# Kernel tuning notes

Measured on AMD Instinct MI355X. Metric: run time of the kernel, lower is better.

## Reference

```python
import jax, jax.numpy as jnp
import numpy as np

# Hyperparameters from init_kwargs
SIGMA = 0.01   # memristor conductance noise std
R = 1.0        # line resistance scale used in power accounting
WMAX1 = 1.0
WMAX2 = 1.0
B, C, H, W = 4, 3, 64, 64
K = 2                      # AvgPool2d kernel/stride
D1 = C * (H // K) * (W // K)   # 3072 flattened features after pooling
D2 = 2048
D3 = 1024


def setup_inputs() -> dict:
    key = jax.random.key(0)
    ks = jax.random.split(key, 4)
    x = jax.random.normal(ks[0], (B, C, H, W), jnp.float32)
    bias = jax.random.normal(ks[1], (C, H, W), jnp.float32) * 0.01
    W1 = jax.random.normal(ks[2], (D2, D1), jnp.float32) / np.float32(np.sqrt(D1))
    W2 = jax.random.normal(ks[3], (D3, D2), jnp.float32) / np.float32(np.sqrt(D2))
    g1 = jnp.float32(1.0)  # learnt_Gmax[0], initialized to Wmax[0]
    g2 = jnp.float32(1.0)  # learnt_Gmax[1]
    return {"x": x, "bias": bias, "W1": W1, "W2": W2, "g1": g1, "g2": g2}


def reference(x, bias, W1, W2, g1, g2):
    # input bias (MemSE.input_bias=True)
    x = x + bias[None]
    b = x.shape[0]
    eye2 = jnp.eye(D2, dtype=x.dtype)
    eye3 = jnp.eye(D3, dtype=x.dtype)

    # --- AvgPool2d(2,2): gamma is still empty at this point, only mean pooled ---
    x = x.reshape(b, C, H // K, K, W // K, K).mean(axis=(3, 5))
    x = x.reshape(b, -1)                        # [B, D1]

    # --- Linear 1: crossbar noise injection (gamma empty -> created here) ---
    c1 = g1 / WMAX1                             # conductance scaling G = c * W
    mu = x @ W1.T                               # [B, D2] mean propagation
    m2 = x * x                                  # E[x^2] (gamma == 0 before this layer)
    # two conductance arrays (pos/neg) each with iid noise var sigma^2, output /c
    vn1 = 2.0 * (SIGMA / c1) ** 2 * jnp.sum(m2, axis=-1)        # [B]
    gamma = vn1[:, None, None] * eye2[None]                      # [B, D2, D2]
    P_tot = (c1 / R) * jnp.einsum('oi,bi->b', jnp.abs(W1), m2)   # crossbar power

    # --- Softplus: first-order moment propagation (Jacobian = sigmoid(mu)) ---
    d = jax.nn.sigmoid(mu)                      # [B, D2]
    gamma = gamma * d[:, :, None] * d[:, None, :]
    mu = jax.nn.softplus(mu)

    # --- Linear 2: full covariance propagation W gamma W^T + noise diag ---
    c2 = g2 / WMAX2
    mu2 = mu @ W2.T                             # [B, D3]
    tmp = jnp.einsum('oi,bij->boj', W2, gamma)  # [B, D3, D2]
    gamma2 = jnp.einsum('boj,pj->bop', tmp, W2) # [B, D3, D3]
    m2b = mu * mu + jnp.diagonal(gamma, axis1=1, axis2=2)        # E[x^2]
    vn2 = 2.0 * (SIGMA / c2) ** 2 * jnp.sum(m2b, axis=-1)
    gamma2 = gamma2 + vn2[:, None, None] * eye3[None]
    P_tot = P_tot + (c2 / R) * jnp.einsum('oi,bi->b', jnp.abs(W2), m2b)

    return mu2, gamma2, P_tot
```

## Files before the change

### kernel.cpp

```cpp
#include <hip/hip_runtime.h>
#include <hip/hip_bf16.h>
#include <cstdint>

#define SIGMA 0.01f

constexpr int D1 = 3072;
constexpr int D2 = 2048;
constexpr int D3 = 1024;

typedef __bf16 bf16x8 __attribute__((ext_vector_type(8)));
typedef float f32x4 __attribute__((ext_vector_type(4)));

#define GLOAD16(gp, lp) \
  __builtin_amdgcn_global_load_lds((const __attribute__((address_space(1))) void*)(gp), \
                                   (__attribute__((address_space(3))) void*)(lp), 16, 0, 0)

__global__ void pool_kernel(const float* __restrict__ x, const float* __restrict__ bias,
                            float* __restrict__ pooled, float* __restrict__ Spart) {
  int idx = blockIdx.x * 256 + threadIdx.x;
  int b = idx / D1;
  int r = idx % D1;
  int c = r >> 10;
  int oh = (r >> 5) & 31;
  int ow = r & 31;
  int xb = ((b * 3 + c) * 64 + oh * 2) * 64 + ow * 2;
  int bb = (c * 64 + oh * 2) * 64 + ow * 2;
  float v = 0.25f * ((x[xb] + bias[bb]) + (x[xb + 1] + bias[bb + 1]) +
                     (x[xb + 64] + bias[bb + 64]) + (x[xb + 65] + bias[bb + 65]));
  pooled[idx] = v;
  float s = v * v;
  #pragma unroll
  for (int off = 32; off; off >>= 1) s += __shfl_down(s, off, 64);
  __shared__ float wsum[4];
  if ((threadIdx.x & 63) == 0) wsum[threadIdx.x >> 6] = s;
  __syncthreads();
  if (threadIdx.x == 0) Spart[blockIdx.x] = wsum[0] + wsum[1] + wsum[2] + wsum[3];
}

__global__ void lin1_kernel(const float* __restrict__ pooled, const float* __restrict__ W1,
                            const float* __restrict__ Spart, const float* __restrict__ g1p,
                            float* __restrict__ musp, float* __restrict__ dscale,
                            float* __restrict__ m2b, float* __restrict__ Pp1) {
  int o = blockIdx.x, tid = threadIdx.x;
  const float4* wrow = (const float4*)(W1 + (size_t)o * D1);
  const float4* p4 = (const float4*)pooled;
  float acc[4] = {0, 0, 0, 0}, pab[4] = {0, 0, 0, 0};
  #pragma unroll
  for (int it = 0; it < 3; it++) {
    int i4 = tid + it * 256;
    float4 w = wrow[i4];
    float ax = fabsf(w.x), ay = fabsf(w.y), az = fabsf(w.z), aw2 = fabsf(w.w);
    #pragma unroll
    for (int b = 0; b < 4; b++) {
      float4 p = p4[b * 768 + i4];
      acc[b] += w.x * p.x + w.y * p.y + w.z * p.z + w.w * p.w;
      pab[b] += ax * p.x * p.x + ay * p.y * p.y + az * p.z * p.z + aw2 * p.w * p.w;
    }
  }
  __shared__ float red[8][4];
  #pragma unroll
  for (int v = 0; v < 8; v++) {
    float s = (v < 4) ? acc[v] : pab[v - 4];
    #pragma unroll
    for (int off = 32; off; off >>= 1) s += __shfl_down(s, off, 64);
    if ((tid & 63) == 0) red[v][tid >> 6] = s;
  }
  __syncthreads();
  if (tid < 8) {
    float s = red[tid][0] + red[tid][1] + red[tid][2] + red[tid][3];
    if (tid < 4) {
      int b = tid;
      float ss = 0.f;
      #pragma unroll
      for (int i = 0; i < 12; i++) ss += Spart[b * 12 + i];
      float c1 = g1p[0];
      float vn1 = 2.0f * (SIGMA / c1) * (SIGMA / c1) * ss;
      float d = 1.0f / (1.0f + expf(-s));
      float sp = fmaxf(s, 0.f) + log1pf(expf(-fabsf(s)));
      musp[b * D2 + o] = sp;
      dscale[b * D2 + o] = sqrtf(vn1) * d;
      m2b[b * D2 + o] = sp * sp + vn1 * d * d;
    } else {
      Pp1[(size_t)(tid - 4) * D2 + o] = s;
    }
  }
}

__global__ void lin2_prep_kernel(const float* __restrict__ W2, const float* __restrict__ musp,
                                 const float* __restrict__ dscale, const float* __restrict__ m2b,
                                 __bf16* __restrict__ E, float* __restrict__ mu2,
                                 float* __restrict__ Pp2) {
  int o = blockIdx.x, tid = threadIdx.x;
  const float* wrow = W2 + (size_t)o * D2;
  int j0 = tid * 8;
  float w[8];
  *(float4*)&w[0] = *(const float4*)(wrow + j0);
  *(float4*)&w[4] = *(const float4*)(wrow + j0 + 4);
  float acc[4], pab[4];
  #pragma unroll
  for (int b = 0; b < 4; b++) {
    const float* ms = musp + b * D2 + j0;
    const float* dsc = dscale + b * D2 + j0;
    const float* mb = m2b + b * D2 + j0;
    bf16x8 ev;
    float a = 0.f, p = 0.f;
    #pragma unroll
    for (int jj = 0; jj < 8; jj++) {
      ev[jj] = (__bf16)(w[jj] * dsc[jj]);
      a += w[jj] * ms[jj];
      p += fabsf(w[jj]) * mb[jj];
    }
    *(bf16x8*)(E + ((size_t)b * D3 + o) * D2 + j0) = ev;
    acc[b] = a;
    pab[b] = p;
  }
  __shared__ float red[8][4];
  #pragma unroll
  for (int v = 0; v < 8; v++) {
    float s = (v < 4) ? acc[v] : pab[v - 4];
    #pragma unroll
    for (int off = 32; off; off >>= 1) s += __shfl_down(s, off, 64);
    if ((tid & 63) == 0) red[v][tid >> 6] = s;
  }
  __syncthreads();
  if (tid < 8) {
    float s = red[tid][0] + red[tid][1] + red[tid][2] + red[tid][3];
    if (tid < 4) mu2[tid * D3 + o] = s;
    else Pp2[(size_t)(tid - 4) * D3 + o] = s;
  }
}

__global__ void scalars_kernel(const float* __restrict__ m2b, const float* __restrict__ Pp1,
                               const float* __restrict__ Pp2, const float* __restrict__ g1p,
                               const float* __restrict__ g2p, float* __restrict__ vn2v,
                               float* __restrict__ Ptot) {
  int b = blockIdx.x, tid = threadIdx.x;
  float sm = 0.f, s1 = 0.f, s2 = 0.f;
  #pragma unroll
  for (int i = 0; i < 8; i++) {
    sm += m2b[(size_t)b * D2 + tid + i * 256];
    s1 += Pp1[(size_t)b * D2 + tid + i * 256];
  }
  #pragma unroll
  for (int i = 0; i < 4; i++) s2 += Pp2[(size_t)b * D3 + tid + i * 256];
  __shared__ float red[3][4];
  #pragma unroll
  for (int v = 0; v < 3; v++) {
    float s = (v == 0) ? sm : (v == 1) ? s1 : s2;
    #pragma unroll
    for (int off = 32; off; off >>= 1) s += __shfl_down(s, off, 64);
    if ((tid & 63) == 0) red[v][tid >> 6] = s;
  }
  __syncthreads();
  if (tid == 0) {
    float c2 = g2p[0];
    float smt = red[0][0] + red[0][1] + red[0][2] + red[0][3];
    float s1t = red[1][0] + red[1][1] + red[1][2] + red[1][3];
    float s2t = red[2][0] + red[2][1] + red[2][2] + red[2][3];
    vn2v[b] = 2.0f * (SIGMA / c2) * (SIGMA / c2) * smt;
    Ptot[b] = g1p[0] * s1t + c2 * s2t;
  }
}

__global__ __launch_bounds__(256, 4) void gamma2_gemm(const __bf16* __restrict__ E,
                                                      const float* __restrict__ vn2v,
                                                      float* __restrict__ gamma2) {
  int bid = blockIdx.x, tid = threadIdx.x;
  int wid = tid >> 6, lane = tid & 63;
  int wr = wid >> 1, wc = wid & 1;

  int xcd = bid & 7, r = bid >> 3;
  int b = xcd >> 1;
  int tm = ((xcd & 1) << 3) | (r & 7);
  int tn = r >> 3;

  __shared__ __bf16 As[2][4096], Bs[2][4096];
  char* AsB = (char*)As;
  char* BsB = (char*)Bs;

  const __bf16* Eb = E + (size_t)b * D3 * D2;
  int rb0 = wid >> 1, ks0 = wid & 1;
  int rb1 = (wid + 4) >> 1, ks1 = wid & 1;
  int srow = lane >> 2, skc = lane & 3;
  const __bf16* gA0 = Eb + (size_t)(tm * 64 + rb0 * 16 + srow) * D2 + ks0 * 32 + skc * 8;
  const __bf16* gA1 = Eb + (size_t)(tm * 64 + rb1 * 16 + srow) * D2 + ks1 * 32 + skc * 8;
  const __bf16* gB0 = Eb + (size_t)(tn * 64 + rb0 * 16 + srow) * D2 + ks0 * 32 + skc * 8;
  const __bf16* gB1 = Eb + (size_t)(tn * 64 + rb1 * 16 + srow) * D2 + ks1 * 32 + skc * 8;
  unsigned dst0 = (unsigned)wid * 1024u;
  unsigned dst1 = dst0 + 4096u;

  int fr = lane & 15, kg = lane >> 4;
  unsigned po = (unsigned)(fr * 64 + kg * 16);
  unsigned aM0 = (unsigned)(wr * 4096) + po;
  unsigned aM1 = aM0 + 2048u;
  unsigned bN0 = (unsigned)(wc * 4096) + po;
  unsigned bN1 = bN0 + 2048u;

  f32x4 acc[2][2] = {};

#define STAGE(bufoff, kelem)                                   \
  {                                                            \
    GLOAD16(gA0 + (kelem), AsB + (bufoff) + dst0);             \
    GLOAD16(gA1 + (kelem), AsB + (bufoff) + dst1);             \
    GLOAD16(gB0 + (kelem), BsB + (bufoff) + dst0);             \
    GLOAD16(gB1 + (kelem), BsB + (bufoff) + dst1);             \
  }

#define COMPUTE(bufoff)                                                         \
  {                                                                             \
    _Pragma("unroll")                                                           \
    for (int ks2 = 0; ks2 < 2; ks2++) {                                         \
      unsigned kso = (unsigned)ks2 << 10;                                       \
      bf16x8 a0 = *(const bf16x8*)(AsB + (bufoff) + aM0 + kso);                 \
      bf16x8 a1 = *(const bf16x8*)(AsB + (bufoff) + aM1 + kso);                 \
      bf16x8 b0 = *(const bf16x8*)(BsB + (bufoff) + bN0 + kso);                 \
      bf16x8 b1 = *(const bf16x8*)(BsB + (bufoff) + bN1 + kso);                 \
      acc[0][0] = __builtin_amdgcn_mfma_f32_16x16x32_bf16(a0, b0, acc[0][0], 0, 0, 0); \
      acc[0][1] = __builtin_amdgcn_mfma_f32_16x16x32_bf16(a0, b1, acc[0][1], 0, 0, 0); \
      acc[1][0] = __builtin_amdgcn_mfma_f32_16x16x32_bf16(a1, b0, acc[1][0], 0, 0, 0); \
      acc[1][1] = __builtin_amdgcn_mfma_f32_16x16x32_bf16(a1, b1, acc[1][1], 0, 0, 0); \
    }                                                                           \
  }

  STAGE(0u, 0);
  __syncthreads();
  unsigned cur = 0;
  #pragma unroll 1
  for (int kt = 0; kt < 31; kt++) {
    unsigned nxt = cur ^ 8192u;
    STAGE(nxt, (kt + 1) * 64);
    COMPUTE(cur);
    __syncthreads();
    cur = nxt;
  }
  COMPUTE(cur);
#undef STAGE
#undef COMPUTE

  float vn2 = vn2v[b];
  float* outb = gamma2 + (size_t)b * D3 * D3;
  int row0 = tm * 64 + wr * 32 + kg * 4;
  int col0 = tn * 64 + wc * 32 + fr;
  #pragma unroll
  for (int mi = 0; mi < 2; mi++)
    #pragma unroll
    for (int ni = 0; ni < 2; ni++)
      #pragma unroll
      for (int rg = 0; rg < 4; rg++) {
        int row = row0 + mi * 16 + rg;
        int cc = col0 + ni * 16;
        float v = acc[mi][ni][rg];
        if (row == cc) v += vn2;
        outb[(size_t)row * D3 + cc] = v;
      }
}

extern "C" void kernel_launch(void* const* d_in, const int* in_sizes, int n_in,
                              void* d_out, int out_size, void* d_ws, size_t ws_size,
                              hipStream_t stream) {
  (void)in_sizes; (void)n_in; (void)out_size; (void)ws_size;
  const float* x    = (const float*)d_in[0];
  const float* bias = (const float*)d_in[1];
  const float* W1   = (const float*)d_in[2];
  const float* W2   = (const float*)d_in[3];
  const float* g1   = (const float*)d_in[4];
  const float* g2   = (const float*)d_in[5];
  float* out = (float*)d_out;

  float* ws     = (float*)d_ws;
  float* pooled = ws;
  float* musp   = pooled + 4 * D1;
  float* dscale = musp + 4 * D2;
  float* m2b    = dscale + 4 * D2;
  float* Pp1    = m2b + 4 * D2;
  float* Pp2    = Pp1 + 4 * D2;
  float* Spart  = Pp2 + 4 * D3;
  float* vn2v   = Spart + 48;
  size_t used = (size_t)(4 * D1 + 4 * 4 * D2 + 4 * D3 + 64) * 4;
  size_t eoff = (used + 255) / 256 * 256;
  __bf16* E = (__bf16*)((char*)d_ws + eoff);

  float* mu2_out  = out;
  float* gam_out  = out + 4 * D3;
  float* ptot_out = out + 4 * D3 + (size_t)4 * D3 * D3;

  pool_kernel<<<48, 256, 0, stream>>>(x, bias, pooled, Spart);
  lin1_kernel<<<2048, 256, 0, stream>>>(pooled, W1, Spart, g1, musp, dscale, m2b, Pp1);
  lin2_prep_kernel<<<1024, 256, 0, stream>>>(W2, musp, dscale, m2b, E, mu2_out, Pp2);
  scalars_kernel<<<4, 256, 0, stream>>>(m2b, Pp1, Pp2, g1, g2, vn2v, ptot_out);
  gamma2_gemm<<<1024, 256, 0, stream>>>(E, vn2v, gam_out);
}
```

Measured before the change: 57.99 us.

## Exploit gamma2 symmetry to compute only upper-triangle tiles; process two rows per block

The covariance GEMM now launches only the upper-triangular 64x64 tiles per batch (136 of 256), decoding tile indices via an inverse triangular-number mapping. Each off-diagonal tile also writes its transposed copy, roughly halving the MFMA work and E-operand loads. In addition, lin1 and lin2_prep each handle two output rows per block, so pooled and activation vectors are reused across rows and fewer blocks are launched. The transposed stores are column-strided float4 writes, which may coalesce poorly.

```diff
diff --git a/kernel.cpp b/kernel.cpp
--- a/kernel.cpp
+++ b/kernel.cpp
@@ -41,35 +41,42 @@
                             const float* __restrict__ Spart, const float* __restrict__ g1p,
                             float* __restrict__ musp, float* __restrict__ dscale,
                             float* __restrict__ m2b, float* __restrict__ Pp1) {
-  int o = blockIdx.x, tid = threadIdx.x;
-  const float4* wrow = (const float4*)(W1 + (size_t)o * D1);
+  int o2 = blockIdx.x << 1, tid = threadIdx.x;
+  const float4* w0p = (const float4*)(W1 + (size_t)o2 * D1);
+  const float4* w1p = (const float4*)(W1 + (size_t)(o2 + 1) * D1);
   const float4* p4 = (const float4*)pooled;
-  float acc[4] = {0, 0, 0, 0}, pab[4] = {0, 0, 0, 0};
+  float a0[4] = {0,0,0,0}, q0[4] = {0,0,0,0}, a1[4] = {0,0,0,0}, q1[4] = {0,0,0,0};
   #pragma unroll
   for (int it = 0; it < 3; it++) {
     int i4 = tid + it * 256;
-    float4 w = wrow[i4];
-    float ax = fabsf(w.x), ay = fabsf(w.y), az = fabsf(w.z), aw2 = fabsf(w.w);
+    float4 w0 = w0p[i4], w1 = w1p[i4];
+    float x0x = fabsf(w0.x), x0y = fabsf(w0.y), x0z = fabsf(w0.z), x0w = fabsf(w0.w);
+    float x1x = fabsf(w1.x), x1y = fabsf(w1.y), x1z = fabsf(w1.z), x1w = fabsf(w1.w);
     #pragma unroll
     for (int b = 0; b < 4; b++) {
       float4 p = p4[b * 768 + i4];
-      acc[b] += w.x * p.x + w.y * p.y + w.z * p.z + w.w * p.w;
-      pab[b] += ax * p.x * p.x + ay * p.y * p.y + az * p.z * p.z + aw2 * p.w * p.w;
+      float px = p.x * p.x, py = p.y * p.y, pz = p.z * p.z, pw = p.w * p.w;
+      a0[b] += w0.x * p.x + w0.y * p.y + w0.z * p.z + w0.w * p.w;
+      q0[b] += x0x * px + x0y * py + x0z * pz + x0w * pw;
+      a1[b] += w1.x * p.x + w1.y * p.y + w1.z * p.z + w1.w * p.w;
+      q1[b] += x1x * px + x1y * py + x1z * pz + x1w * pw;
     }
   }
-  __shared__ float red[8][4];
-  #pragma unroll
-  for (int v = 0; v < 8; v++) {
-    float s = (v < 4) ? acc[v] : pab[v - 4];
+  __shared__ float red[16][4];
+  #pragma unroll
+  for (int v = 0; v < 16; v++) {
+    float s = (v < 4) ? a0[v] : (v < 8) ? q0[v - 4] : (v < 12) ? a1[v - 8] : q1[v - 12];
     #pragma unroll
     for (int off = 32; off; off >>= 1) s += __shfl_down(s, off, 64);
     if ((tid & 63) == 0) red[v][tid >> 6] = s;
   }
   __syncthreads();
-  if (tid < 8) {
+  if (tid < 16) {
     float s = red[tid][0] + red[tid][1] + red[tid][2] + red[tid][3];
-    if (tid < 4) {
-      int b = tid;
+    int rr = tid >> 3, u = tid & 7;
+    int o = o2 + rr;
+    if (u < 4) {
+      int b = u;
       float ss = 0.f;
       #pragma unroll
       for (int i = 0; i < 12; i++) ss += Spart[b * 12 + i];
@@ -81,7 +88,7 @@
       dscale[b * D2 + o] = sqrtf(vn1) * d;
       m2b[b * D2 + o] = sp * sp + vn1 * d * d;
     } else {
-      Pp1[(size_t)(tid - 4) * D2 + o] = s;
+      Pp1[(size_t)(u - 4) * D2 + o] = s;
     }
   }
 }
@@ -90,43 +97,48 @@
                                  const float* __restrict__ dscale, const float* __restrict__ m2b,
                                  __bf16* __restrict__ E, float* __restrict__ mu2,
                                  float* __restrict__ Pp2) {
-  int o = blockIdx.x, tid = threadIdx.x;
-  const float* wrow = W2 + (size_t)o * D2;
+  int o2 = blockIdx.x << 1, tid = threadIdx.x;
   int j0 = tid * 8;
-  float w[8];
-  *(float4*)&w[0] = *(const float4*)(wrow + j0);
-  *(float4*)&w[4] = *(const float4*)(wrow + j0 + 4);
-  float acc[4], pab[4];
+  float w0[8], w1[8];
+  *(float4*)&w0[0] = *(const float4*)(W2 + (size_t)o2 * D2 + j0);
+  *(float4*)&w0[4] = *(const float4*)(W2 + (size_t)o2 * D2 + j0 + 4);
+  *(float4*)&w1[0] = *(const float4*)(W2 + (size_t)(o2 + 1) * D2 + j0);
+  *(float4*)&w1[4] = *(const float4*)(W2 + (size_t)(o2 + 1) * D2 + j0 + 4);
+  float a0[4], q0[4], a1[4], q1[4];
   #pragma unroll
   for (int b = 0; b < 4; b++) {
     const float* ms = musp + b * D2 + j0;
     const float* dsc = dscale + b * D2 + j0;
     const float* mb = m2b + b * D2 + j0;
-    bf16x8 ev;
-    float a = 0.f, p = 0.f;
+    bf16x8 e0, e1;
+    float s0 = 0.f, p0 = 0.f, s1 = 0.f, p1 = 0.f;
     #pragma unroll
     for (int jj = 0; jj < 8; jj++) {
-      ev[jj] = (__bf16)(w[jj] * dsc[jj]);
-      a += w[jj] * ms[jj];
-      p += fabsf(w[jj]) * mb[jj];
+      float dv = dsc[jj], mv = ms[jj], bv = mb[jj];
+      e0[jj] = (__bf16)(w0[jj] * dv);
+      e1[jj] = (__bf16)(w1[jj] * dv);
+      s0 += w0[jj] * mv;  p0 += fabsf(w0[jj]) * bv;
+      s1 += w1[jj] * mv;  p1 += fabsf(w1[jj]) * bv;
     }
-    *(bf16x8*)(E + ((size_t)b * D3 + o) * D2 + j0) = ev;
-    acc[b] = a;
-    pab[b] = p;
-  }
-  __shared__ float red[8][4];
-  #pragma unroll
-  for (int v = 0; v < 8; v++) {
-    float s = (v < 4) ? acc[v] : pab[v - 4];
+    *(bf16x8*)(E + ((size_t)b * D3 + o2) * D2 + j0) = e0;
+    *(bf16x8*)(E + ((size_t)b * D3 + o2 + 1) * D2 + j0) = e1;
+    a0[b] = s0; q0[b] = p0; a1[b] = s1; q1[b] = p1;
+  }
+  __shared__ float red[16][4];
+  #pragma unroll
+  for (int v = 0; v < 16; v++) {
+    float s = (v < 4) ? a0[v] : (v < 8) ? q0[v - 4] : (v < 12) ? a1[v - 8] : q1[v - 12];
     #pragma unroll
     for (int off = 32; off; off >>= 1) s += __shfl_down(s, off, 64);
     if ((tid & 63) == 0) red[v][tid >> 6] = s;
   }
   __syncthreads();
-  if (tid < 8) {
+  if (tid < 16) {
     float s = red[tid][0] + red[tid][1] + red[tid][2] + red[tid][3];
-    if (tid < 4) mu2[tid * D3 + o] = s;
-    else Pp2[(size_t)(tid - 4) * D3 + o] = s;
+    int rr = tid >> 3, u = tid & 7;
+    int o = o2 + rr;
+    if (u < 4) mu2[u * D3 + o] = s;
+    else Pp2[(size_t)(u - 4) * D3 + o] = s;
   }
 }
 
@@ -171,8 +183,13 @@
 
   int xcd = bid & 7, r = bid >> 3;
   int b = xcd >> 1;
-  int tm = ((xcd & 1) << 3) | (r & 7);
-  int tn = r >> 3;
+  int t = (r << 1) | (xcd & 1);
+  int s = 135 - t;
+  int k = (int)((sqrtf((float)(8 * s + 1)) - 1.0f) * 0.5f);
+  while ((k + 1) * (k + 2) / 2 <= s) k++;
+  while (k * (k + 1) / 2 > s) k--;
+  int i = s - k * (k + 1) / 2;
+  int tm = 15 - k, tn = 15 - i;
 
   __shared__ __bf16 As[2][4096], Bs[2][4096];
   char* AsB = (char*)As;
@@ -180,12 +197,12 @@
 
   const __bf16* Eb = E + (size_t)b * D3 * D2;
   int rb0 = wid >> 1, ks0 = wid & 1;
-  int rb1 = (wid + 4) >> 1, ks1 = wid & 1;
+  int rb1 = (wid + 4) >> 1;
   int srow = lane >> 2, skc = lane & 3;
   const __bf16* gA0 = Eb + (size_t)(tm * 64 + rb0 * 16 + srow) * D2 + ks0 * 32 + skc * 8;
-  const __bf16* gA1 = Eb + (size_t)(tm * 64 + rb1 * 16 + srow) * D2 + ks1 * 32 + skc * 8;
+  const __bf16* gA1 = Eb + (size_t)(tm * 64 + rb1 * 16 + srow) * D2 + ks0 * 32 + skc * 8;
   const __bf16* gB0 = Eb + (size_t)(tn * 64 + rb0 * 16 + srow) * D2 + ks0 * 32 + skc * 8;
-  const __bf16* gB1 = Eb + (size_t)(tn * 64 + rb1 * 16 + srow) * D2 + ks1 * 32 + skc * 8;
+  const __bf16* gB1 = Eb + (size_t)(tn * 64 + rb1 * 16 + srow) * D2 + ks0 * 32 + skc * 8;
   unsigned dst0 = (unsigned)wid * 1024u;
   unsigned dst1 = dst0 + 4096u;
 
@@ -253,6 +270,16 @@
         if (row == cc) v += vn2;
         outb[(size_t)row * D3 + cc] = v;
       }
+  if (tm != tn) {
+    #pragma unroll
+    for (int mi = 0; mi < 2; mi++)
+      #pragma unroll
+      for (int ni = 0; ni < 2; ni++) {
+        int cc = col0 + ni * 16;
+        int rowb = row0 + mi * 16;
+        *(f32x4*)(outb + (size_t)cc * D3 + rowb) = acc[mi][ni];
+      }
+  }
 }
 
 extern "C" void kernel_launch(void* const* d_in, const int* in_sizes, int n_in,
@@ -285,8 +312,8 @@
   float* ptot_out = out + 4 * D3 + (size_t)4 * D3 * D3;
 
   pool_kernel<<<48, 256, 0, stream>>>(x, bias, pooled, Spart);
-  lin1_kernel<<<2048, 256, 0, stream>>>(pooled, W1, Spart, g1, musp, dscale, m2b, Pp1);
-  lin2_prep_kernel<<<1024, 256, 0, stream>>>(W2, musp, dscale, m2b, E, mu2_out, Pp2);
+  lin1_kernel<<<1024, 256, 0, stream>>>(pooled, W1, Spart, g1, musp, dscale, m2b, Pp1);
+  lin2_prep_kernel<<<512, 256, 0, stream>>>(W2, musp, dscale, m2b, E, mu2_out, Pp2);
   scalars_kernel<<<4, 256, 0, stream>>>(m2b, Pp1, Pp2, g1, g2, vn2v, ptot_out);
-  gamma2_gemm<<<1024, 256, 0, stream>>>(E, vn2v, gam_out);
-}
+  gamma2_gemm<<<544, 256, 0, stream>>>(E, vn2v, gam_out);
+}
```

Result: faster. 56.41 us (-2.7%).
